# Kernel optimization log

Measured on AMD Instinct MI355X. Metric: run time of the kernel, lower is better.

The kernel has to match this reference:

```python
import jax, jax.numpy as jnp
import numpy as np

TOPK = 1
NUM_STAT = 3

def setup_inputs() -> dict:
    key = jax.random.key(0)
    ks = jax.random.split(key, 12)
    L, B, D, R, E, RD = 2048, 8, 1024, 8, 2, 8
    H = D // 2
    s = 0.02
    inp = {
        'x': jax.random.normal(ks[0], (L, B, D), jnp.float32),
        'missing_embed': jax.random.uniform(ks[1], (B, RD), jnp.float32),
        'A_dyn': jax.random.normal(ks[2], (E, D, R), jnp.float32) * s,
        'B_dyn': jax.random.normal(ks[3], (E, R, D), jnp.float32) * s,
        'W1': jax.random.normal(ks[4], (D + RD, H), jnp.float32) * (1.0 / np.sqrt(D + RD)),
        'b1': jnp.zeros((H,), jnp.float32),
        'W2': jax.random.normal(ks[5], (H, E), jnp.float32) * (1.0 / np.sqrt(H)),
        'b2': jnp.zeros((E,), jnp.float32),
        'A_stat': jax.random.normal(ks[6], (NUM_STAT, D, R), jnp.float32) * s,
        'B_stat': jax.random.normal(ks[7], (NUM_STAT, R, D), jnp.float32) * s,
        'Wout': jax.random.normal(ks[8], (D, D), jnp.float32) * (1.0 / np.sqrt(D)),
        'bout': jnp.zeros((D,), jnp.float32),
    }
    return inp


def reference(x, missing_embed, A_dyn, B_dyn, W1, b1, W2, b2, A_stat, B_stat, Wout, bout):
    L, B, D = x.shape
    E = A_dyn.shape[0]
    # router: gates over dynamic experts
    m = jnp.broadcast_to(missing_embed[None], (L, B, missing_embed.shape[-1]))
    h = jax.nn.gelu(jnp.concatenate([x, m], axis=-1) @ W1 + b1, approximate=False)
    gates = jax.nn.softmax(h @ W2 + b2, axis=-1)          # [L,B,E]
    topv, topi = jax.lax.top_k(gates, TOPK)               # [L,B,TOPK]
    # per-expert dynamic LoRA deltas: x @ A_e @ B_e  -> [E,L,B,D]
    deltas = jnp.einsum('lbr,erd->elbd', jnp.einsum('lbd,edr->lbr' if False else 'lbd,edr->lber', x, A_dyn).transpose(0,1,3,2).reshape(L,B,-1).reshape(L,B,E,-1).transpose(0,1,2,3), B_dyn) if False else jnp.einsum('lber,erd->elbd', jnp.einsum('lbd,edr->lber', x, A_dyn), B_dyn)
    # combine: weight per expert = sum_i topv_i * (topi_i == e)
    onehot = jax.nn.one_hot(topi, E, dtype=x.dtype)        # [L,B,TOPK,E]
    w = jnp.einsum('lbt,lbte->lbe', topv, onehot)          # [L,B,E]
    dyn = jnp.einsum('lbe,elbd->lbd', w, deltas)
    # static LoRAs
    shared = (x @ A_stat[0]) @ B_stat[0]
    act = (missing_embed[:, 1:NUM_STAT] > 0.5).astype(x.dtype)  # [B, NUM_STAT-1]
    spec_deltas = jnp.einsum('lbjr,jrd->jlbd', jnp.einsum('lbd,jdr->lbjr', x, A_stat[1:]), B_stat[1:])
    spec = jnp.einsum('bj,jlbd->lbd', act, spec_deltas)
    delta_h = jax.nn.gelu(dyn + shared + spec, approximate=False) @ Wout + bout
    return delta_h
```

## Files before the change

kernel.cpp:

```cpp
#include <hip/hip_runtime.h>
#include <hip/hip_bf16.h>


typedef __attribute__((ext_vector_type(4))) float f32x4;
typedef __attribute__((ext_vector_type(8))) short bf16x8;
typedef __attribute__((ext_vector_type(8))) unsigned short u16x8;

__device__ __forceinline__ float geluf(float v) {
    return 0.5f * v * (1.0f + erff(v * 0.70710678118654752440f));
}
__device__ __forceinline__ unsigned short f2bf(float v) {
    return __builtin_bit_cast(unsigned short, __float2bfloat16(v));
}
__device__ __forceinline__ float bf2f(unsigned short u) {
    unsigned int x = ((unsigned int)u) << 16;
    return __builtin_bit_cast(float, x);
}
__device__ __forceinline__ void gload16(const void* g, void* l) {
    __builtin_amdgcn_global_load_lds(
        (const __attribute__((address_space(1))) unsigned int*)g,
        (__attribute__((address_space(3))) unsigned int*)l, 16, 0, 0);
}

__global__ void kprep(const float* __restrict__ me, const float* __restrict__ W1,
                      const float* __restrict__ b1, float* __restrict__ Cb,
                      float* __restrict__ actb) {
    int h = threadIdx.x;
    for (int b = 0; b < 8; b++) {
        float s = b1[h];
        #pragma unroll
        for (int r = 0; r < 8; r++) s += me[b * 8 + r] * W1[(1024 + r) * 512 + h];
        Cb[b * 512 + h] = s;
    }
    if (h < 16) {
        int b = h >> 1, j = h & 1;
        actb[b * 2 + j] = (me[b * 8 + 1 + j] > 0.5f) ? 1.0f : 0.0f;
    }
}

__global__ void kwout(const float* __restrict__ Wout, unsigned short* __restrict__ WT) {
    __shared__ float s[32][33];
    const int blk = blockIdx.x;
    const int kt = blk >> 5, nt = blk & 31;
    const int r = threadIdx.x >> 3, c4 = (threadIdx.x & 7) * 4;
    f32x4 v = *(const f32x4*)(Wout + (size_t)(kt * 32 + r) * 1024 + nt * 32 + c4);
    s[r][c4 + 0] = v[0]; s[r][c4 + 1] = v[1]; s[r][c4 + 2] = v[2]; s[r][c4 + 3] = v[3];
    __syncthreads();
    const int n = r, kc = c4;
    ushort4 o;
    o.x = f2bf(s[kc + 0][n]); o.y = f2bf(s[kc + 1][n]);
    o.z = f2bf(s[kc + 2][n]); o.w = f2bf(s[kc + 3][n]);
    *(ushort4*)(WT + (size_t)(nt * 32 + n) * 1024 + kt * 32 + kc) = o;
}

__global__ void kwsplit(const float* __restrict__ W1, const float* __restrict__ A_dyn,
                        const float* __restrict__ A_stat,
                        unsigned short* __restrict__ WThi, unsigned short* __restrict__ WTlo) {
    __shared__ float s[32][33];
    const int nt = blockIdx.x >> 5;
    const int kt = blockIdx.x & 31;
    const int r = threadIdx.x >> 3;
    const int c4 = (threadIdx.x & 7) * 4;
    const int k = kt * 32 + r;
    if (nt < 16) {
        f32x4 v = *(const f32x4*)(W1 + (size_t)k * 512 + nt * 32 + c4);
        s[r][c4 + 0] = v[0]; s[r][c4 + 1] = v[1];
        s[r][c4 + 2] = v[2]; s[r][c4 + 3] = v[3];
    } else {
        #pragma unroll
        for (int j = 0; j < 4; j++) {
            int ng = nt * 32 + c4 + j;
            float val = 0.f;
            if (ng < 552) {
                int mi = (ng - 512) >> 3, rr = (ng - 512) & 7;
                const float* Ab = (mi < 2) ? (A_dyn + (size_t)mi * 8192)
                                           : (A_stat + (size_t)(mi - 2) * 8192);
                val = Ab[(size_t)k * 8 + rr];
            }
            s[r][c4 + j] = val;
        }
    }
    __syncthreads();
    ushort4 oh, ol;
    float f0 = s[c4 + 0][r], f1 = s[c4 + 1][r], f2 = s[c4 + 2][r], f3 = s[c4 + 3][r];
    oh.x = f2bf(f0); ol.x = f2bf(f0 - bf2f(oh.x));
    oh.y = f2bf(f1); ol.y = f2bf(f1 - bf2f(oh.y));
    oh.z = f2bf(f2); ol.z = f2bf(f2 - bf2f(oh.z));
    oh.w = f2bf(f3); ol.w = f2bf(f3 - bf2f(oh.w));
    size_t obase = (size_t)(nt * 32 + r) * 1024 + kt * 32 + c4;
    *(ushort4*)(WThi + obase) = oh;
    *(ushort4*)(WTlo + obase) = ol;
}

__launch_bounds__(256)
__global__ void krouterg(const float* __restrict__ x,
                         const unsigned short* __restrict__ WThi,
                         const unsigned short* __restrict__ WTlo,
                         const float* __restrict__ Cb,
                         const float* __restrict__ W2,
                         float* __restrict__ plog,
                         float* __restrict__ r_raw) {
    __shared__ unsigned short xhi[128 * 32], xlo[128 * 32];
    __shared__ unsigned short bhi_s[128 * 32], blo_s[128 * 32];
    __shared__ float plw[4][64][2];

    const int tid = threadIdx.x;
    const int lane = tid & 63;
    const int wave = tid >> 6;
    const int nt = blockIdx.x % 5;
    const int mb = blockIdx.x / 5;
    const int m0 = mb * 128, n0 = nt * 128;
    const int wm = wave >> 1, wn = wave & 1;

    f32x4 acc[4][4];
    #pragma unroll
    for (int i = 0; i < 4; i++)
        #pragma unroll
        for (int j = 0; j < 4; j++) acc[i][j] = f32x4{0.f, 0.f, 0.f, 0.f};

    const int sr = tid >> 1;
    const int sc = (tid & 1) * 16;
    const float* xsrc = x + (size_t)(m0 + sr) * 1024 + sc;
    const int swz = (sr >> 1) & 3;
    const int st0 = sr * 32 + (((sc >> 3) + 0) ^ swz) * 8;
    const int st1 = sr * 32 + (((sc >> 3) + 1) ^ swz) * 8;

    int brow[2], bsl[2], bofs[2];
    #pragma unroll
    for (int i = 0; i < 2; i++) {
        int ldsbyte = i * 4096 + tid * 16;
        int row = ldsbyte >> 6;
        int ss = (ldsbyte >> 4) & 3;
        brow[i] = row;
        bsl[i] = ss ^ ((row >> 1) & 3);
        bofs[i] = ldsbyte >> 1;
    }

    int aoff[4], boff[4];
    #pragma unroll
    for (int f = 0; f < 4; f++) {
        int rA = 64 * wm + 16 * f + (lane & 15);
        aoff[f] = rA * 32 + (((lane >> 4) ^ ((rA >> 1) & 3)) * 8);
        int rB = 64 * wn + 16 * f + (lane & 15);
        boff[f] = rB * 32 + (((lane >> 4) ^ ((rB >> 1) & 3)) * 8);
    }

    for (int k0 = 0; k0 < 1024; k0 += 32) {
        __syncthreads();
        #pragma unroll
        for (int i = 0; i < 2; i++) {
            const unsigned short* g1 = WThi + (size_t)(n0 + brow[i]) * 1024 + k0 + bsl[i] * 8;
            gload16(g1, &bhi_s[bofs[i]]);
            const unsigned short* g2 = WTlo + (size_t)(n0 + brow[i]) * 1024 + k0 + bsl[i] * 8;
            gload16(g2, &blo_s[bofs[i]]);
        }
        f32x4 v0 = *(const f32x4*)(xsrc + 0);
        f32x4 v1 = *(const f32x4*)(xsrc + 4);
        f32x4 v2 = *(const f32x4*)(xsrc + 8);
        f32x4 v3 = *(const f32x4*)(xsrc + 12);
        xsrc += 32;
        u16x8 h0, l0v, h1, l1v;
        #pragma unroll
        for (int j = 0; j < 4; j++) {
            float f = v0[j]; unsigned short hs = f2bf(f);
            h0[j] = hs; l0v[j] = f2bf(f - bf2f(hs));
            f = v1[j]; hs = f2bf(f);
            h0[4 + j] = hs; l0v[4 + j] = f2bf(f - bf2f(hs));
            f = v2[j]; hs = f2bf(f);
            h1[j] = hs; l1v[j] = f2bf(f - bf2f(hs));
            f = v3[j]; hs = f2bf(f);
            h1[4 + j] = hs; l1v[4 + j] = f2bf(f - bf2f(hs));
        }
        *(u16x8*)&xhi[st0] = h0; *(u16x8*)&xlo[st0] = l0v;
        *(u16x8*)&xhi[st1] = h1; *(u16x8*)&xlo[st1] = l1v;
        __syncthreads();
        bf16x8 ah[4], al[4], bh[4], bl[4];
        #pragma unroll
        for (int f = 0; f < 4; f++) {
            ah[f] = *(const bf16x8*)&xhi[aoff[f]];
            al[f] = *(const bf16x8*)&xlo[aoff[f]];
            bh[f] = *(const bf16x8*)&bhi_s[boff[f]];
            bl[f] = *(const bf16x8*)&blo_s[boff[f]];
        }
        #pragma unroll
        for (int fi = 0; fi < 4; fi++)
            #pragma unroll
            for (int fj = 0; fj < 4; fj++) {
                acc[fi][fj] = __builtin_amdgcn_mfma_f32_16x16x32_bf16(ah[fi], bh[fj], acc[fi][fj], 0, 0, 0);
                acc[fi][fj] = __builtin_amdgcn_mfma_f32_16x16x32_bf16(ah[fi], bl[fj], acc[fi][fj], 0, 0, 0);
                acc[fi][fj] = __builtin_amdgcn_mfma_f32_16x16x32_bf16(al[fi], bh[fj], acc[fi][fj], 0, 0, 0);
            }
    }

    if (nt < 4) {
        #pragma unroll
        for (int fi = 0; fi < 4; fi++) {
            #pragma unroll
            for (int q = 0; q < 4; q++) {
                const int b = (((lane >> 4) * 4 + q) & 7);
                float s0 = 0.f, s1 = 0.f;
                #pragma unroll
                for (int fj = 0; fj < 4; fj++) {
                    int col = n0 + 64 * wn + 16 * fj + (lane & 15);
                    float val = acc[fi][fj][q] + Cb[b * 512 + col];
                    float hv = geluf(val);
                    s0 += hv * W2[col * 2];
                    s1 += hv * W2[col * 2 + 1];
                }
                #pragma unroll
                for (int off = 1; off < 16; off <<= 1) {
                    s0 += __shfl_xor(s0, off, 16);
                    s1 += __shfl_xor(s1, off, 16);
                }
                if ((lane & 15) == 0) {
                    int rloc = 16 * fi + (lane >> 4) * 4 + q;
                    plw[wave][rloc][0] = s0;
                    plw[wave][rloc][1] = s1;
                }
            }
        }
        __syncthreads();
        {
            int row = tid >> 1, e = tid & 1;
            float tot = plw[(row >> 6) * 2][row & 63][e] + plw[(row >> 6) * 2 + 1][row & 63][e];
            plog[((size_t)nt * 16384 + m0 + row) * 2 + e] = tot;
        }
    } else {
        if (wn == 0) {
            #pragma unroll
            for (int fi = 0; fi < 4; fi++)
                #pragma unroll
                for (int fj = 0; fj < 3; fj++) {
                    int col = 16 * fj + (lane & 15);
                    if (col < 40) {
                        #pragma unroll
                        for (int q = 0; q < 4; q++) {
                            int row = 64 * wm + 16 * fi + (lane >> 4) * 4 + q;
                            r_raw[(size_t)(m0 + row) * 40 + col] = acc[fi][fj][q];
                        }
                    }
                }
        }
    }
}

__launch_bounds__(256)
__global__ void kgates(const float* __restrict__ plog, const float* __restrict__ b2,
                       const float* __restrict__ x, const float* __restrict__ W1,
                       const float* __restrict__ Cb, const float* __restrict__ W2,
                       float* __restrict__ gates) {
    const int tid = threadIdx.x;
    const int t = blockIdx.x * 256 + tid;
    float l0 = b2[0], l1 = b2[1];
    #pragma unroll
    for (int p = 0; p < 4; p++) {
        l0 += plog[((size_t)p * 16384 + t) * 2];
        l1 += plog[((size_t)p * 16384 + t) * 2 + 1];
    }
    __shared__ int list[256];
    __shared__ float fixv[256][2];
    __shared__ int cnt;
    __shared__ float xrow[1024];
    __shared__ float wred[4][2];
    if (tid == 0) cnt = 0;
    __syncthreads();
    int myi = -1;
    if (fabsf(l0 - l1) < 1e-3f) myi = atomicAdd(&cnt, 1);
    if (myi >= 0) list[myi] = tid;
    __syncthreads();
    const int n = cnt;
    for (int ii = 0; ii < n; ii++) {
        __syncthreads();
        const int lt = list[ii];
        const int tok = blockIdx.x * 256 + lt;
        for (int c = tid; c < 1024; c += 256) xrow[c] = x[(size_t)tok * 1024 + c];
        __syncthreads();
        const int b = tok & 7;
        float pre0 = Cb[b * 512 + tid], pre1 = Cb[b * 512 + tid + 256];
        for (int k = 0; k < 1024; k++) {
            const float xv = xrow[k];
            pre0 += xv * W1[k * 512 + tid];
            pre1 += xv * W1[k * 512 + tid + 256];
        }
        float hv0 = geluf(pre0), hv1 = geluf(pre1);
        float s0 = hv0 * W2[tid * 2] + hv1 * W2[(tid + 256) * 2];
        float s1 = hv0 * W2[tid * 2 + 1] + hv1 * W2[(tid + 256) * 2 + 1];
        #pragma unroll
        for (int off = 1; off < 64; off <<= 1) {
            s0 += __shfl_xor(s0, off, 64);
            s1 += __shfl_xor(s1, off, 64);
        }
        if ((tid & 63) == 0) { wred[tid >> 6][0] = s0; wred[tid >> 6][1] = s1; }
        __syncthreads();
        if (tid == 0) {
            fixv[ii][0] = wred[0][0] + wred[1][0] + wred[2][0] + wred[3][0] + b2[0];
            fixv[ii][1] = wred[0][1] + wred[1][1] + wred[2][1] + wred[3][1] + b2[1];
        }
    }
    __syncthreads();
    if (myi >= 0) { l0 = fixv[myi][0]; l1 = fixv[myi][1]; }
    float topv = 1.f / (1.f + expf(-fabsf(l0 - l1)));
    gates[(size_t)t * 2]     = (l0 >= l1) ? topv : 0.f;
    gates[(size_t)t * 2 + 1] = (l0 >= l1) ? 0.f : topv;
}

__global__ void kdelta(const float* __restrict__ r_raw, const float* __restrict__ gates,
                       const float* __restrict__ actb,
                       const float* __restrict__ B_dyn, const float* __restrict__ B_stat,
                       unsigned short* __restrict__ z) {
    __shared__ float rl[16 * 40];
    const int tid = threadIdx.x;
    const int t0 = blockIdx.x * 16;
    for (int f = tid; f < 640; f += 256) {
        const int tt = t0 + f / 40, j = f % 40, mi = j >> 3;
        float w;
        if (mi == 0) w = gates[(size_t)tt * 2];
        else if (mi == 1) w = gates[(size_t)tt * 2 + 1];
        else if (mi == 2) w = 1.f;
        else w = actb[(tt & 7) * 2 + (mi - 3)];
        rl[f] = w * r_raw[(size_t)tt * 40 + j];
    }
    __syncthreads();
    const int c0 = tid * 4;
    f32x4 acc[16];
    #pragma unroll
    for (int t = 0; t < 16; t++) acc[t] = f32x4{0.f, 0.f, 0.f, 0.f};
    for (int i = 0; i < 40; i++) {
        const float* Brow = (i < 16) ? (B_dyn + (size_t)i * 1024)
                                     : (B_stat + (size_t)(i - 16) * 1024);
        f32x4 b4 = *(const f32x4*)(Brow + c0);
        #pragma unroll
        for (int t = 0; t < 16; t++) acc[t] += b4 * rl[t * 40 + i];
    }
    #pragma unroll
    for (int t = 0; t < 16; t++) {
        f32x4 v = acc[t];
        ushort4 o;
        o.x = f2bf(geluf(v[0])); o.y = f2bf(geluf(v[1]));
        o.z = f2bf(geluf(v[2])); o.w = f2bf(geluf(v[3]));
        *(ushort4*)(z + (size_t)(t0 + t) * 1024 + c0) = o;
    }
}

__launch_bounds__(256, 2)
__global__ void kgemm(const unsigned short* __restrict__ z,
                      const unsigned short* __restrict__ WT,
                      const float* __restrict__ bout, float* __restrict__ out) {
    __shared__ unsigned short lA[128 * 32];
    __shared__ unsigned short lB[128 * 32];
    const int tid = threadIdx.x;
    const int lane = tid & 63;
    const int wave = tid >> 6;
    const int m0 = (blockIdx.x >> 3) * 128;
    const int n0 = (blockIdx.x & 7) * 128;
    const int wm = wave >> 1, wn = wave & 1;

    f32x4 acc[4][4];
    #pragma unroll
    for (int i = 0; i < 4; i++)
        #pragma unroll
        for (int j = 0; j < 4; j++) acc[i][j] = f32x4{0.f, 0.f, 0.f, 0.f};

    for (int k0 = 0; k0 < 1024; k0 += 32) {
        __syncthreads();
        #pragma unroll
        for (int q = 0; q < 2; q++) {
            int c = tid + 256 * q;
            int row = c >> 2, ss = c & 3;
            int sl = ss ^ ((row >> 1) & 3);
            f32x4 va = *(const f32x4*)(z + (size_t)(m0 + row) * 1024 + k0 + sl * 8);
            *(f32x4*)&lA[row * 32 + ss * 8] = va;
            f32x4 vb = *(const f32x4*)(WT + (size_t)(n0 + row) * 1024 + k0 + sl * 8);
            *(f32x4*)&lB[row * 32 + ss * 8] = vb;
        }
        __syncthreads();
        bf16x8 af[4], bfr[4];
        #pragma unroll
        for (int fi = 0; fi < 4; fi++) {
            int rA = 64 * wm + 16 * fi + (lane & 15);
            int sl = (lane >> 4) ^ ((rA >> 1) & 3);
            af[fi] = *(const bf16x8*)&lA[rA * 32 + sl * 8];
        }
        #pragma unroll
        for (int fj = 0; fj < 4; fj++) {
            int rB = 64 * wn + 16 * fj + (lane & 15);
            int sl = (lane >> 4) ^ ((rB >> 1) & 3);
            bfr[fj] = *(const bf16x8*)&lB[rB * 32 + sl * 8];
        }
        #pragma unroll
        for (int fi = 0; fi < 4; fi++)
            #pragma unroll
            for (int fj = 0; fj < 4; fj++)
                acc[fi][fj] = __builtin_amdgcn_mfma_f32_16x16x32_bf16(
                    af[fi], bfr[fj], acc[fi][fj], 0, 0, 0);
    }
    #pragma unroll
    for (int fj = 0; fj < 4; fj++) {
        int n = n0 + 64 * wn + 16 * fj + (lane & 15);
        float bo = bout[n];
        #pragma unroll
        for (int fi = 0; fi < 4; fi++) {
            int mr = m0 + 64 * wm + 16 * fi + (lane >> 4) * 4;
            #pragma unroll
            for (int q = 0; q < 4; q++)
                out[(size_t)(mr + q) * 1024 + n] = acc[fi][fj][q] + bo;
        }
    }
}

extern "C" void kernel_launch(void* const* d_in, const int* in_sizes, int n_in,
                              void* d_out, int out_size, void* d_ws, size_t ws_size,
                              hipStream_t stream) {
    const float* x      = (const float*)d_in[0];
    const float* me     = (const float*)d_in[1];
    const float* A_dyn  = (const float*)d_in[2];
    const float* B_dyn  = (const float*)d_in[3];
    const float* W1     = (const float*)d_in[4];
    const float* b1     = (const float*)d_in[5];
    const float* W2     = (const float*)d_in[6];
    const float* b2     = (const float*)d_in[7];
    const float* A_stat = (const float*)d_in[8];
    const float* B_stat = (const float*)d_in[9];
    const float* Wout   = (const float*)d_in[10];
    const float* bout   = (const float*)d_in[11];
    float* out = (float*)d_out;

    char* ws = (char*)d_ws;
    float*          Cb    = (float*)(ws + 0);
    float*          actb  = (float*)(ws + 16384);
    unsigned short* WT    = (unsigned short*)(ws + 65536);
    unsigned short* WThi  = (unsigned short*)(ws + 2162688);
    unsigned short* WTlo  = (unsigned short*)(ws + 3473408);
    float*          plog  = (float*)(ws + 4784128);
    float*          gates = (float*)(ws + 5308416);
    float*          r_raw = (float*)(ws + 5439488);
    unsigned short* z     = (unsigned short*)(ws + 8060928);

    kprep<<<1, 512, 0, stream>>>(me, W1, b1, Cb, actb);
    kwout<<<1024, 256, 0, stream>>>(Wout, WT);
    kwsplit<<<640, 256, 0, stream>>>(W1, A_dyn, A_stat, WThi, WTlo);
    krouterg<<<640, 256, 0, stream>>>(x, WThi, WTlo, Cb, W2, plog, r_raw);
    kgates<<<64, 256, 0, stream>>>(plog, b2, x, W1, Cb, W2, gates);
    kdelta<<<1024, 256, 0, stream>>>(r_raw, gates, actb, B_dyn, B_stat, z);
    kgemm<<<1024, 256, 0, stream>>>(z, WT, bout, out);
}
```

Measured before the change: 416.8 us.

## Drop x low-part split in router GEMM and spread near-tie fixups globally

Adds a pre-pass that converts x to a single bf16 copy, so the router GEMM loads x through direct global-to-LDS copies and issues two MFMAs per tile instead of three, skipping the low-part B MFMAs for the LoRA-rank tile. To offset the lost precision, the near-tie threshold for exact fp32 recomputation is widened, and the fixup moves into a separate kernel that takes tokens from a global atomic list spread across 128 blocks. The extra conversion pass writes a 32MB bf16 copy of x, and more tokens fall into the recompute path.

New measurement: 375.3 us. -9.9%, faster.

```diff
diff --git a/kernel.cpp b/kernel.cpp
--- a/kernel.cpp
+++ b/kernel.cpp
@@ -24,7 +24,7 @@
 
 __global__ void kprep(const float* __restrict__ me, const float* __restrict__ W1,
                       const float* __restrict__ b1, float* __restrict__ Cb,
-                      float* __restrict__ actb) {
+                      float* __restrict__ actb, int* __restrict__ fixcnt) {
     int h = threadIdx.x;
     for (int b = 0; b < 8; b++) {
         float s = b1[h];
@@ -36,6 +36,7 @@
         int b = h >> 1, j = h & 1;
         actb[b * 2 + j] = (me[b * 8 + 1 + j] > 0.5f) ? 1.0f : 0.0f;
     }
+    if (h == 0) *fixcnt = 0;
 }
 
 __global__ void kwout(const float* __restrict__ Wout, unsigned short* __restrict__ WT) {
@@ -92,16 +93,25 @@
     *(ushort4*)(WTlo + obase) = ol;
 }
 
+__global__ void kxbf(const float* __restrict__ x, unsigned short* __restrict__ xh) {
+    const size_t i = ((size_t)blockIdx.x * 256 + threadIdx.x) * 8;
+    f32x4 a = *(const f32x4*)(x + i);
+    f32x4 b = *(const f32x4*)(x + i + 4);
+    u16x8 o;
+    o[0] = f2bf(a[0]); o[1] = f2bf(a[1]); o[2] = f2bf(a[2]); o[3] = f2bf(a[3]);
+    o[4] = f2bf(b[0]); o[5] = f2bf(b[1]); o[6] = f2bf(b[2]); o[7] = f2bf(b[3]);
+    *(u16x8*)(xh + i) = o;
+}
+
 __launch_bounds__(256)
-__global__ void krouterg(const float* __restrict__ x,
+__global__ void krouterg(const unsigned short* __restrict__ xh,
                          const unsigned short* __restrict__ WThi,
                          const unsigned short* __restrict__ WTlo,
                          const float* __restrict__ Cb,
                          const float* __restrict__ W2,
                          float* __restrict__ plog,
                          float* __restrict__ r_raw) {
-    __shared__ unsigned short xhi[128 * 32], xlo[128 * 32];
-    __shared__ unsigned short bhi_s[128 * 32], blo_s[128 * 32];
+    __shared__ unsigned short xs[128 * 32], bhs[128 * 32], bls[128 * 32];
     __shared__ float plw[4][64][2];
 
     const int tid = threadIdx.x;
@@ -111,6 +121,7 @@
     const int mb = blockIdx.x / 5;
     const int m0 = mb * 128, n0 = nt * 128;
     const int wm = wave >> 1, wn = wave & 1;
+    const bool rtile = (nt == 4);
 
     f32x4 acc[4][4];
     #pragma unroll
@@ -118,22 +129,15 @@
         #pragma unroll
         for (int j = 0; j < 4; j++) acc[i][j] = f32x4{0.f, 0.f, 0.f, 0.f};
 
-    const int sr = tid >> 1;
-    const int sc = (tid & 1) * 16;
-    const float* xsrc = x + (size_t)(m0 + sr) * 1024 + sc;
-    const int swz = (sr >> 1) & 3;
-    const int st0 = sr * 32 + (((sc >> 3) + 0) ^ swz) * 8;
-    const int st1 = sr * 32 + (((sc >> 3) + 1) ^ swz) * 8;
-
-    int brow[2], bsl[2], bofs[2];
+    int srow[2], ssl[2], sofs[2];
     #pragma unroll
     for (int i = 0; i < 2; i++) {
         int ldsbyte = i * 4096 + tid * 16;
         int row = ldsbyte >> 6;
         int ss = (ldsbyte >> 4) & 3;
-        brow[i] = row;
-        bsl[i] = ss ^ ((row >> 1) & 3);
-        bofs[i] = ldsbyte >> 1;
+        srow[i] = row;
+        ssl[i] = ss ^ ((row >> 1) & 3);
+        sofs[i] = ldsbyte >> 1;
     }
 
     int aoff[4], boff[4];
@@ -145,54 +149,47 @@
         boff[f] = rB * 32 + (((lane >> 4) ^ ((rB >> 1) & 3)) * 8);
     }
 
+    const unsigned short* xb = xh + (size_t)m0 * 1024;
+    const unsigned short* bhb = WThi + (size_t)n0 * 1024;
+    const unsigned short* blb = WTlo + (size_t)n0 * 1024;
+
     for (int k0 = 0; k0 < 1024; k0 += 32) {
         __syncthreads();
         #pragma unroll
         for (int i = 0; i < 2; i++) {
-            const unsigned short* g1 = WThi + (size_t)(n0 + brow[i]) * 1024 + k0 + bsl[i] * 8;
-            gload16(g1, &bhi_s[bofs[i]]);
-            const unsigned short* g2 = WTlo + (size_t)(n0 + brow[i]) * 1024 + k0 + bsl[i] * 8;
-            gload16(g2, &blo_s[bofs[i]]);
-        }
-        f32x4 v0 = *(const f32x4*)(xsrc + 0);
-        f32x4 v1 = *(const f32x4*)(xsrc + 4);
-        f32x4 v2 = *(const f32x4*)(xsrc + 8);
-        f32x4 v3 = *(const f32x4*)(xsrc + 12);
-        xsrc += 32;
-        u16x8 h0, l0v, h1, l1v;
-        #pragma unroll
-        for (int j = 0; j < 4; j++) {
-            float f = v0[j]; unsigned short hs = f2bf(f);
-            h0[j] = hs; l0v[j] = f2bf(f - bf2f(hs));
-            f = v1[j]; hs = f2bf(f);
-            h0[4 + j] = hs; l0v[4 + j] = f2bf(f - bf2f(hs));
-            f = v2[j]; hs = f2bf(f);
-            h1[j] = hs; l1v[j] = f2bf(f - bf2f(hs));
-            f = v3[j]; hs = f2bf(f);
-            h1[4 + j] = hs; l1v[4 + j] = f2bf(f - bf2f(hs));
-        }
-        *(u16x8*)&xhi[st0] = h0; *(u16x8*)&xlo[st0] = l0v;
-        *(u16x8*)&xhi[st1] = h1; *(u16x8*)&xlo[st1] = l1v;
-        __syncthreads();
-        bf16x8 ah[4], al[4], bh[4], bl[4];
+            const size_t go = (size_t)srow[i] * 1024 + k0 + ssl[i] * 8;
+            gload16(xb + go, &xs[sofs[i]]);
+            gload16(bhb + go, &bhs[sofs[i]]);
+            if (!rtile) gload16(blb + go, &bls[sofs[i]]);
+        }
+        __syncthreads();
+        bf16x8 ah[4], bh[4];
         #pragma unroll
         for (int f = 0; f < 4; f++) {
-            ah[f] = *(const bf16x8*)&xhi[aoff[f]];
-            al[f] = *(const bf16x8*)&xlo[aoff[f]];
-            bh[f] = *(const bf16x8*)&bhi_s[boff[f]];
-            bl[f] = *(const bf16x8*)&blo_s[boff[f]];
-        }
-        #pragma unroll
-        for (int fi = 0; fi < 4; fi++)
-            #pragma unroll
-            for (int fj = 0; fj < 4; fj++) {
-                acc[fi][fj] = __builtin_amdgcn_mfma_f32_16x16x32_bf16(ah[fi], bh[fj], acc[fi][fj], 0, 0, 0);
-                acc[fi][fj] = __builtin_amdgcn_mfma_f32_16x16x32_bf16(ah[fi], bl[fj], acc[fi][fj], 0, 0, 0);
-                acc[fi][fj] = __builtin_amdgcn_mfma_f32_16x16x32_bf16(al[fi], bh[fj], acc[fi][fj], 0, 0, 0);
-            }
-    }
-
-    if (nt < 4) {
+            ah[f] = *(const bf16x8*)&xs[aoff[f]];
+            bh[f] = *(const bf16x8*)&bhs[boff[f]];
+        }
+        if (!rtile) {
+            bf16x8 bl[4];
+            #pragma unroll
+            for (int f = 0; f < 4; f++) bl[f] = *(const bf16x8*)&bls[boff[f]];
+            #pragma unroll
+            for (int fi = 0; fi < 4; fi++)
+                #pragma unroll
+                for (int fj = 0; fj < 4; fj++) {
+                    acc[fi][fj] = __builtin_amdgcn_mfma_f32_16x16x32_bf16(ah[fi], bh[fj], acc[fi][fj], 0, 0, 0);
+                    acc[fi][fj] = __builtin_amdgcn_mfma_f32_16x16x32_bf16(ah[fi], bl[fj], acc[fi][fj], 0, 0, 0);
+                }
+        } else if (wn == 0) {
+            #pragma unroll
+            for (int fi = 0; fi < 4; fi++)
+                #pragma unroll
+                for (int fj = 0; fj < 3; fj++)
+                    acc[fi][fj] = __builtin_amdgcn_mfma_f32_16x16x32_bf16(ah[fi], bh[fj], acc[fi][fj], 0, 0, 0);
+        }
+    }
+
+    if (!rtile) {
         #pragma unroll
         for (int fi = 0; fi < 4; fi++) {
             #pragma unroll
@@ -244,35 +241,37 @@
     }
 }
 
-__launch_bounds__(256)
 __global__ void kgates(const float* __restrict__ plog, const float* __restrict__ b2,
-                       const float* __restrict__ x, const float* __restrict__ W1,
-                       const float* __restrict__ Cb, const float* __restrict__ W2,
-                       float* __restrict__ gates) {
-    const int tid = threadIdx.x;
-    const int t = blockIdx.x * 256 + tid;
+                       float* __restrict__ gates, int* __restrict__ fixlist,
+                       int* __restrict__ fixcnt) {
+    const int t = blockIdx.x * 256 + threadIdx.x;
     float l0 = b2[0], l1 = b2[1];
     #pragma unroll
     for (int p = 0; p < 4; p++) {
         l0 += plog[((size_t)p * 16384 + t) * 2];
         l1 += plog[((size_t)p * 16384 + t) * 2 + 1];
     }
-    __shared__ int list[256];
-    __shared__ float fixv[256][2];
-    __shared__ int cnt;
+    if (fabsf(l0 - l1) < 8e-3f) {
+        int i = atomicAdd(fixcnt, 1);
+        fixlist[i] = t;
+    }
+    float topv = 1.f / (1.f + expf(-fabsf(l0 - l1)));
+    gates[(size_t)t * 2]     = (l0 >= l1) ? topv : 0.f;
+    gates[(size_t)t * 2 + 1] = (l0 >= l1) ? 0.f : topv;
+}
+
+__launch_bounds__(256)
+__global__ void kfix(const int* __restrict__ fixlist, const int* __restrict__ fixcnt,
+                     const float* __restrict__ x, const float* __restrict__ W1,
+                     const float* __restrict__ Cb, const float* __restrict__ W2,
+                     const float* __restrict__ b2, float* __restrict__ gates) {
     __shared__ float xrow[1024];
     __shared__ float wred[4][2];
-    if (tid == 0) cnt = 0;
-    __syncthreads();
-    int myi = -1;
-    if (fabsf(l0 - l1) < 1e-3f) myi = atomicAdd(&cnt, 1);
-    if (myi >= 0) list[myi] = tid;
-    __syncthreads();
-    const int n = cnt;
-    for (int ii = 0; ii < n; ii++) {
-        __syncthreads();
-        const int lt = list[ii];
-        const int tok = blockIdx.x * 256 + lt;
+    const int tid = threadIdx.x;
+    const int n = *fixcnt;
+    for (int i = blockIdx.x; i < n; i += gridDim.x) {
+        const int tok = fixlist[i];
+        __syncthreads();
         for (int c = tid; c < 1024; c += 256) xrow[c] = x[(size_t)tok * 1024 + c];
         __syncthreads();
         const int b = tok & 7;
@@ -282,9 +281,9 @@
             pre0 += xv * W1[k * 512 + tid];
             pre1 += xv * W1[k * 512 + tid + 256];
         }
-        float hv0 = geluf(pre0), hv1 = geluf(pre1);
-        float s0 = hv0 * W2[tid * 2] + hv1 * W2[(tid + 256) * 2];
-        float s1 = hv0 * W2[tid * 2 + 1] + hv1 * W2[(tid + 256) * 2 + 1];
+        float h0 = geluf(pre0), h1 = geluf(pre1);
+        float s0 = h0 * W2[tid * 2] + h1 * W2[(tid + 256) * 2];
+        float s1 = h0 * W2[tid * 2 + 1] + h1 * W2[(tid + 256) * 2 + 1];
         #pragma unroll
         for (int off = 1; off < 64; off <<= 1) {
             s0 += __shfl_xor(s0, off, 64);
@@ -293,15 +292,14 @@
         if ((tid & 63) == 0) { wred[tid >> 6][0] = s0; wred[tid >> 6][1] = s1; }
         __syncthreads();
         if (tid == 0) {
-            fixv[ii][0] = wred[0][0] + wred[1][0] + wred[2][0] + wred[3][0] + b2[0];
-            fixv[ii][1] = wred[0][1] + wred[1][1] + wred[2][1] + wred[3][1] + b2[1];
-        }
-    }
-    __syncthreads();
-    if (myi >= 0) { l0 = fixv[myi][0]; l1 = fixv[myi][1]; }
-    float topv = 1.f / (1.f + expf(-fabsf(l0 - l1)));
-    gates[(size_t)t * 2]     = (l0 >= l1) ? topv : 0.f;
-    gates[(size_t)t * 2 + 1] = (l0 >= l1) ? 0.f : topv;
+            float l0 = wred[0][0] + wred[1][0] + wred[2][0] + wred[3][0] + b2[0];
+            float l1 = wred[0][1] + wred[1][1] + wred[2][1] + wred[3][1] + b2[1];
+            float topv = 1.f / (1.f + expf(-fabsf(l0 - l1)));
+            gates[(size_t)tok * 2]     = (l0 >= l1) ? topv : 0.f;
+            gates[(size_t)tok * 2 + 1] = (l0 >= l1) ? 0.f : topv;
+        }
+        __syncthreads();
+    }
 }
 
 __global__ void kdelta(const float* __restrict__ r_raw, const float* __restrict__ gates,
@@ -426,21 +424,26 @@
     float* out = (float*)d_out;
 
     char* ws = (char*)d_ws;
-    float*          Cb    = (float*)(ws + 0);
-    float*          actb  = (float*)(ws + 16384);
-    unsigned short* WT    = (unsigned short*)(ws + 65536);
-    unsigned short* WThi  = (unsigned short*)(ws + 2162688);
-    unsigned short* WTlo  = (unsigned short*)(ws + 3473408);
-    float*          plog  = (float*)(ws + 4784128);
-    float*          gates = (float*)(ws + 5308416);
-    float*          r_raw = (float*)(ws + 5439488);
-    unsigned short* z     = (unsigned short*)(ws + 8060928);
-
-    kprep<<<1, 512, 0, stream>>>(me, W1, b1, Cb, actb);
+    float*          Cb     = (float*)(ws + 0);
+    float*          actb   = (float*)(ws + 16384);
+    int*            fixcnt = (int*)(ws + 16448);
+    unsigned short* WT     = (unsigned short*)(ws + 65536);
+    unsigned short* WThi   = (unsigned short*)(ws + 2162688);
+    unsigned short* WTlo   = (unsigned short*)(ws + 3473408);
+    float*          plog   = (float*)(ws + 4784128);
+    float*          gates  = (float*)(ws + 5308416);
+    float*          r_raw  = (float*)(ws + 5439488);
+    int*            fixlist= (int*)(ws + 8060928);
+    unsigned short* xh     = (unsigned short*)(ws + 8126464);
+    unsigned short* z      = (unsigned short*)(ws + 41680896);
+
+    kprep<<<1, 512, 0, stream>>>(me, W1, b1, Cb, actb, fixcnt);
     kwout<<<1024, 256, 0, stream>>>(Wout, WT);
     kwsplit<<<640, 256, 0, stream>>>(W1, A_dyn, A_stat, WThi, WTlo);
-    krouterg<<<640, 256, 0, stream>>>(x, WThi, WTlo, Cb, W2, plog, r_raw);
-    kgates<<<64, 256, 0, stream>>>(plog, b2, x, W1, Cb, W2, gates);
+    kxbf<<<8192, 256, 0, stream>>>(x, xh);
+    krouterg<<<640, 256, 0, stream>>>(xh, WThi, WTlo, Cb, W2, plog, r_raw);
+    kgates<<<64, 256, 0, stream>>>(plog, b2, gates, fixlist, fixcnt);
+    kfix<<<128, 256, 0, stream>>>(fixlist, fixcnt, x, W1, Cb, W2, b2, gates);
     kdelta<<<1024, 256, 0, stream>>>(r_raw, gates, actb, B_dyn, B_stat, z);
     kgemm<<<1024, 256, 0, stream>>>(z, WT, bout, out);
 }
```
